# Kernel optimization log

Hardware: AMD Instinct MI355X
Metric: run time of the kernel (lower is better)

The kernel has to match this reference:

```python
import jax, jax.numpy as jnp
import numpy as np

B, S, D, H = 16, 2048, 1024, 1024

def setup_inputs() -> dict:
    key = jax.random.key(0)
    k1, k2, k3 = jax.random.split(key, 3)
    X = jax.random.normal(k1, (B, S, D), dtype=jnp.float32)
    W = jax.random.normal(k2, (3 * H, D), dtype=jnp.float32) * (1.0 / np.sqrt(D))
    b = jax.random.normal(k3, (3 * H,), dtype=jnp.float32) * 0.01
    return {"X": X, "W": W, "b": b}

def forget_mult(z, f):
    # z, f: [B, S, H]; h_t = z_t * f_t + (1 - f_t) * h_{t-1}, h_{-1} = 0
    z_t = jnp.moveaxis(z, 1, 0)  # [S, B, H]
    f_t = jnp.moveaxis(f, 1, 0)
    h0 = jnp.zeros(z.shape[::2], dtype=z.dtype)  # [B, H]
    def step(h, zf):
        zt, ft = zf
        h = zt * ft + (1.0 - ft) * h
        return h, h
    _, cs = jax.lax.scan(step, h0, (z_t, f_t))
    return jnp.moveaxis(cs, 0, 1)  # [B, S, H]

def reference(X, W, b):
    # window=1, output_gate=True, batch_first=True, zoneout=0, hidden=None
    Y = jnp.einsum('bsd,ed->bse', X, W) + b  # [B, S, 3H]
    z_gate, f_gate, o_gate = jnp.split(Y, 3, axis=2)
    z_gate = jnp.tanh(z_gate)
    f_gate = jax.nn.sigmoid(f_gate)
    c_gate = forget_mult(z_gate, f_gate)
    output = jax.nn.sigmoid(o_gate) * c_gate
    return output, c_gate[:, -1:]
```

## Files before the change

### kernel.cpp

```cpp
#include <hip/hip_runtime.h>
#include <hip/hip_bf16.h>
#include <hip/hip_fp16.h>


#define BB 16
#define SS 2048
#define DD 1024
#define HH 1024
#define N3 3072
#define CHUNK 64
#define NC (SS/CHUNK)

typedef _Float16 f16x8 __attribute__((ext_vector_type(8)));
typedef float    f32x4 __attribute__((ext_vector_type(4)));

__device__ __forceinline__ float sigm_f(float x) {
    return 1.0f / (1.0f + __expf(-x));
}
__device__ __forceinline__ float tanh_f(float x) {
    float ax = fabsf(x);
    float e  = __expf(2.0f * ax);
    float r  = 1.0f - 2.0f / (e + 1.0f);
    return copysignf(r, x);
}

__global__ __launch_bounds__(256) void cvt_f32_f16(
    const float* __restrict__ src, __half* __restrict__ dst, int n8)
{
    int i = blockIdx.x * 256 + threadIdx.x;
    if (i >= n8) return;
    const float4* s = (const float4*)src + (size_t)i * 2;
    float4 a = s[0], b = s[1];
    f16x8 v;
    v[0] = (_Float16)a.x; v[1] = (_Float16)a.y; v[2] = (_Float16)a.z; v[3] = (_Float16)a.w;
    v[4] = (_Float16)b.x; v[5] = (_Float16)b.y; v[6] = (_Float16)b.z; v[7] = (_Float16)b.w;
    *((f16x8*)dst + i) = v;
}

__global__ __launch_bounds__(256) void gemm_gates(
    const __half* __restrict__ Xs,
    const __half* __restrict__ W16,
    const float*  __restrict__ bias,
    __half* __restrict__ G)
{
    __shared__ __half As[128 * 32] __attribute__((aligned(16)));
    __shared__ __half Bs[128 * 32] __attribute__((aligned(16)));

    const int t  = threadIdx.x;
    const int w  = t >> 6;
    const int l  = t & 63;
    const int m0 = blockIdx.y * 128;
    const int n0 = blockIdx.x * 128;
    const int wm = w >> 1;
    const int wn = w & 1;

    f32x4 acc[4][4];
    #pragma unroll
    for (int m = 0; m < 4; ++m)
        #pragma unroll
        for (int n = 0; n < 4; ++n)
            acc[m][n] = f32x4{0.f, 0.f, 0.f, 0.f};

    const int c0 = w;
    const int c1 = w + 4;
    const int rA0 = c0 * 16 + (l >> 2);
    const int rA1 = c1 * 16 + (l >> 2);
    const int ck  = (l & 3) * 8;

    const __half* Xb = Xs + (size_t)m0 * DD;
    const __half* Wb = W16 + (size_t)n0 * DD;

    const int cl = l & 15;
    const int kg = l >> 4;

    for (int k0 = 0; k0 < DD; k0 += 32) {
        __builtin_amdgcn_global_load_lds(
            (const __attribute__((address_space(1))) void*)(Xb + (size_t)rA0 * DD + k0 + ck),
            (__attribute__((address_space(3))) void*)((char*)As + c0 * 1024), 16, 0, 0);
        __builtin_amdgcn_global_load_lds(
            (const __attribute__((address_space(1))) void*)(Xb + (size_t)rA1 * DD + k0 + ck),
            (__attribute__((address_space(3))) void*)((char*)As + c1 * 1024), 16, 0, 0);
        __builtin_amdgcn_global_load_lds(
            (const __attribute__((address_space(1))) void*)(Wb + (size_t)rA0 * DD + k0 + ck),
            (__attribute__((address_space(3))) void*)((char*)Bs + c0 * 1024), 16, 0, 0);
        __builtin_amdgcn_global_load_lds(
            (const __attribute__((address_space(1))) void*)(Wb + (size_t)rA1 * DD + k0 + ck),
            (__attribute__((address_space(3))) void*)((char*)Bs + c1 * 1024), 16, 0, 0);
        __syncthreads();

        f16x8 a[4], b[4];
        const f16x8* Av = (const f16x8*)As;
        const f16x8* Bv = (const f16x8*)Bs;
        #pragma unroll
        for (int m = 0; m < 4; ++m)
            a[m] = Av[(wm * 64 + m * 16 + cl) * 4 + kg];
        #pragma unroll
        for (int n = 0; n < 4; ++n)
            b[n] = Bv[(wn * 64 + n * 16 + cl) * 4 + kg];

        #pragma unroll
        for (int m = 0; m < 4; ++m)
            #pragma unroll
            for (int n = 0; n < 4; ++n)
                acc[m][n] = __builtin_amdgcn_mfma_f32_16x16x32_f16(
                    a[m], b[n], acc[m][n], 0, 0, 0);
        __syncthreads();
    }

    #pragma unroll
    for (int n = 0; n < 4; ++n) {
        const int gcol = n0 + wn * 64 + n * 16 + cl;
        const float bv = bias[gcol];
        #pragma unroll
        for (int m = 0; m < 4; ++m) {
            const int grow0 = m0 + wm * 64 + m * 16 + kg * 4;
            #pragma unroll
            for (int i = 0; i < 4; ++i) {
                G[(size_t)(grow0 + i) * N3 + gcol] = __float2half(acc[m][n][i] + bv);
            }
        }
    }
}

__global__ __launch_bounds__(256) void scan_pass1(
    const __half* __restrict__ G,
    float* __restrict__ Ac, float* __restrict__ Fc)
{
    const int flat = blockIdx.x * 256 + threadIdx.x;
    const int h  = flat & (HH - 1);
    const int c  = (flat >> 10) & (NC - 1);
    const int lb = flat >> 15;

    const __half* g = G + (size_t)(lb * SS + c * CHUNK) * N3 + h;
    float A = 0.f, F = 1.f;
    for (int s = 0; s < CHUNK; ++s) {
        float z = __half2float(g[0]);
        float f = __half2float(g[HH]);
        g += N3;
        float ft = sigm_f(f);
        float fp = 1.f - ft;
        A = tanh_f(z) * ft + fp * A;
        F *= fp;
    }
    Ac[flat] = A;
    Fc[flat] = F;
}

__global__ __launch_bounds__(256) void scan_pass2(
    const float* __restrict__ Ac, const float* __restrict__ Fc,
    float* __restrict__ Hin, float* __restrict__ c_last)
{
    const int flat = blockIdx.x * 256 + threadIdx.x;
    const int lb = flat >> 10;
    const int h  = flat & (HH - 1);
    float hc = 0.f;
    for (int c = 0; c < NC; ++c) {
        const size_t idx = (size_t)(lb * NC + c) * HH + h;
        Hin[idx] = hc;
        hc = Ac[idx] + Fc[idx] * hc;
    }
    c_last[flat] = hc;
}

__global__ __launch_bounds__(256) void scan_pass3(
    const __half* __restrict__ G, const float* __restrict__ Hin,
    float* __restrict__ out)
{
    const int flat = blockIdx.x * 256 + threadIdx.x;
    const int h  = flat & (HH - 1);
    const int c  = (flat >> 10) & (NC - 1);
    const int lb = flat >> 15;

    const __half* g = G + (size_t)(lb * SS + c * CHUNK) * N3 + h;
    float* o = out + (size_t)(lb * SS + c * CHUNK) * HH + h;
    float hc = Hin[flat];
    for (int s = 0; s < CHUNK; ++s) {
        float z  = __half2float(g[0]);
        float f  = __half2float(g[HH]);
        float og = __half2float(g[2 * HH]);
        g += N3;
        float ft = sigm_f(f);
        hc = tanh_f(z) * ft + (1.f - ft) * hc;
        *o = hc * sigm_f(og);
        o += HH;
    }
}

extern "C" void kernel_launch(void* const* d_in, const int* in_sizes, int n_in,
                              void* d_out, int out_size, void* d_ws, size_t ws_size,
                              hipStream_t stream) {
    const float* X    = (const float*)d_in[0];
    const float* W    = (const float*)d_in[1];
    const float* bias = (const float*)d_in[2];
    for (int i = 0; i < n_in && i < 3; ++i) {
        if      (in_sizes[i] == BB * SS * DD) X    = (const float*)d_in[i];
        else if (in_sizes[i] == N3 * DD)      W    = (const float*)d_in[i];
        else if (in_sizes[i] == N3)           bias = (const float*)d_in[i];
    }
    float* out = (float*)d_out;
    float* c_last_base = out + (size_t)BB * SS * HH;

    const size_t w16_b   = (size_t)N3 * DD * sizeof(__half);
    const size_t per_b_x = (size_t)SS * DD * sizeof(__half);
    const size_t per_b_g = (size_t)SS * N3 * sizeof(__half);
    const size_t per_b_s = (size_t)NC * HH * sizeof(float) * 3;
    int nb = 1;
    for (int cand = BB; cand >= 1; --cand) {
        if (w16_b + (size_t)cand * (per_b_x + per_b_g + per_b_s) <= ws_size) {
            nb = cand; break;
        }
    }

    __half* W16 = (__half*)d_ws;
    __half* X16 = (__half*)((char*)W16 + w16_b);
    __half* G   = (__half*)((char*)X16 + (size_t)nb * per_b_x);
    float*  Ac  = (float*)((char*)G + (size_t)nb * per_b_g);
    float*  Fc  = Ac + (size_t)nb * NC * HH;
    float*  Hin = Fc + (size_t)nb * NC * HH;

    {
        const int n8 = (N3 * DD) / 8;
        cvt_f32_f16<<<(n8 + 255) / 256, 256, 0, stream>>>(W, W16, n8);
    }

    for (int b0 = 0; b0 < BB; b0 += nb) {
        const int bs = (b0 + nb <= BB) ? nb : (BB - b0);

        const int n8x = (bs * SS * DD) / 8;
        cvt_f32_f16<<<(n8x + 255) / 256, 256, 0, stream>>>(
            X + (size_t)b0 * SS * DD, X16, n8x);

        dim3 gg(N3 / 128, bs * (SS / 128));
        gemm_gates<<<gg, 256, 0, stream>>>(X16, W16, bias, G);

        scan_pass1<<<(bs * NC * HH) / 256, 256, 0, stream>>>(G, Ac, Fc);
        scan_pass2<<<(bs * HH) / 256, 256, 0, stream>>>(Ac, Fc, Hin,
                                                        c_last_base + (size_t)b0 * HH);
        scan_pass3<<<(bs * NC * HH) / 256, 256, 0, stream>>>(G, Hin,
                                                             out + (size_t)b0 * SS * HH);
    }
}
```

Measured before the change: 425.6 us.

## Rewrite gate GEMM as 256x256x64 double-buffered 8-wave pipelined kernel

Replaces the 128x128x32 single-buffered GEMM with a 256x256 tile, BK=64, 512-thread kernel. It double-buffers LDS with async global-to-LDS loads that are split across phases, so the next tile's loads overlap the MFMA work. It also adds s_setprio, sched barriers and a swapped grid order so M-blocks vary fastest. The aim is to raise arithmetic intensity and hide memory latency in the dominant GEMM, at the cost of more LDS (128KB), more registers and reduced occupancy, plus a risk of LDS bank conflicts because the layout is unswizzled.

Measured after the change: 638.9 us. 50.1% more time.

```diff
diff --git a/kernel.cpp b/kernel.cpp
--- a/kernel.cpp
+++ b/kernel.cpp
@@ -10,6 +10,11 @@
 #define N3 3072
 #define CHUNK 64
 #define NC (SS/CHUNK)
+
+#define BM 256
+#define BN 256
+#define BK 64
+#define NKT (DD/BK)
 
 typedef _Float16 f16x8 __attribute__((ext_vector_type(8)));
 typedef float    f32x4 __attribute__((ext_vector_type(4)));
@@ -37,86 +42,120 @@
     *((f16x8*)dst + i) = v;
 }
 
-__global__ __launch_bounds__(256) void gemm_gates(
+__global__ __launch_bounds__(512) void gemm_gates8(
     const __half* __restrict__ Xs,
     const __half* __restrict__ W16,
     const float*  __restrict__ bias,
     __half* __restrict__ G)
 {
-    __shared__ __half As[128 * 32] __attribute__((aligned(16)));
-    __shared__ __half Bs[128 * 32] __attribute__((aligned(16)));
-
-    const int t  = threadIdx.x;
-    const int w  = t >> 6;
-    const int l  = t & 63;
-    const int m0 = blockIdx.y * 128;
-    const int n0 = blockIdx.x * 128;
-    const int wm = w >> 1;
-    const int wn = w & 1;
-
-    f32x4 acc[4][4];
+    __shared__ __half As[2][BM * BK] __attribute__((aligned(16)));
+    __shared__ __half Bs[2][BN * BK] __attribute__((aligned(16)));
+
+    const int t   = threadIdx.x;
+    const int wid = t >> 6;
+    const int l   = t & 63;
+    const int m0  = blockIdx.x * BM;
+    const int n0  = blockIdx.y * BN;
+    const int wr  = wid >> 2;
+    const int wc  = wid & 3;
+    const int cl  = l & 15;
+    const int kg  = l >> 4;
+
+    f32x4 acc[8][4];
     #pragma unroll
-    for (int m = 0; m < 4; ++m)
+    for (int m = 0; m < 8; ++m)
         #pragma unroll
         for (int n = 0; n < 4; ++n)
             acc[m][n] = f32x4{0.f, 0.f, 0.f, 0.f};
 
-    const int c0 = w;
-    const int c1 = w + 4;
-    const int rA0 = c0 * 16 + (l >> 2);
-    const int rA1 = c1 * 16 + (l >> 2);
-    const int ck  = (l & 3) * 8;
-
-    const __half* Xb = Xs + (size_t)m0 * DD;
-    const __half* Wb = W16 + (size_t)n0 * DD;
-
-    const int cl = l & 15;
-    const int kg = l >> 4;
-
-    for (int k0 = 0; k0 < DD; k0 += 32) {
-        __builtin_amdgcn_global_load_lds(
-            (const __attribute__((address_space(1))) void*)(Xb + (size_t)rA0 * DD + k0 + ck),
-            (__attribute__((address_space(3))) void*)((char*)As + c0 * 1024), 16, 0, 0);
-        __builtin_amdgcn_global_load_lds(
-            (const __attribute__((address_space(1))) void*)(Xb + (size_t)rA1 * DD + k0 + ck),
-            (__attribute__((address_space(3))) void*)((char*)As + c1 * 1024), 16, 0, 0);
-        __builtin_amdgcn_global_load_lds(
-            (const __attribute__((address_space(1))) void*)(Wb + (size_t)rA0 * DD + k0 + ck),
-            (__attribute__((address_space(3))) void*)((char*)Bs + c0 * 1024), 16, 0, 0);
-        __builtin_amdgcn_global_load_lds(
-            (const __attribute__((address_space(1))) void*)(Wb + (size_t)rA1 * DD + k0 + ck),
-            (__attribute__((address_space(3))) void*)((char*)Bs + c1 * 1024), 16, 0, 0);
-        __syncthreads();
-
-        f16x8 a[4], b[4];
-        const f16x8* Av = (const f16x8*)As;
-        const f16x8* Bv = (const f16x8*)Bs;
-        #pragma unroll
-        for (int m = 0; m < 4; ++m)
-            a[m] = Av[(wm * 64 + m * 16 + cl) * 4 + kg];
-        #pragma unroll
-        for (int n = 0; n < 4; ++n)
-            b[n] = Bv[(wn * 64 + n * 16 + cl) * 4 + kg];
-
-        #pragma unroll
-        for (int m = 0; m < 4; ++m)
-            #pragma unroll
-            for (int n = 0; n < 4; ++n)
-                acc[m][n] = __builtin_amdgcn_mfma_f32_16x16x32_f16(
-                    a[m], b[n], acc[m][n], 0, 0, 0);
-        __syncthreads();
-    }
+    const int srow = wid * 8 + (l >> 3);
+    const int scol = (l & 7) * 8;
+    const __half* Xb = Xs  + (size_t)(m0 + srow) * DD + scol;
+    const __half* Wb = W16 + (size_t)(n0 + srow) * DD + scol;
+
+#define ISSUE_A(slot, j, kt) \
+    __builtin_amdgcn_global_load_lds( \
+        (const __attribute__((address_space(1))) void*)(Xb + (size_t)(j) * 64 * DD + (kt) * BK), \
+        (__attribute__((address_space(3))) void*)(&As[slot][(j) * 4096 + wid * 512]), 16, 0, 0)
+#define ISSUE_B(slot, j, kt) \
+    __builtin_amdgcn_global_load_lds( \
+        (const __attribute__((address_space(1))) void*)(Wb + (size_t)(j) * 64 * DD + (kt) * BK), \
+        (__attribute__((address_space(3))) void*)(&Bs[slot][(j) * 4096 + wid * 512]), 16, 0, 0)
+
+#define PHASE(q, EXTRA) { \
+        const int rh = (q) >> 1, ch = (q) & 1; \
+        f16x8 a[4][2], b[2][2]; \
+        _Pragma("unroll") \
+        for (int i = 0; i < 4; ++i) \
+            _Pragma("unroll") \
+            for (int kh = 0; kh < 2; ++kh) \
+                a[i][kh] = *(const f16x8*)(Ab + ((wr * 128 + (rh * 4 + i) * 16 + cl) * BK + kh * 32 + kg * 8)); \
+        _Pragma("unroll") \
+        for (int j = 0; j < 2; ++j) \
+            _Pragma("unroll") \
+            for (int kh = 0; kh < 2; ++kh) \
+                b[j][kh] = *(const f16x8*)(Bb + ((wc * 64 + (ch * 2 + j) * 16 + cl) * BK + kh * 32 + kg * 8)); \
+        EXTRA; \
+        __builtin_amdgcn_s_barrier(); \
+        asm volatile("s_waitcnt lgkmcnt(0)" ::: "memory"); \
+        __builtin_amdgcn_sched_barrier(0); \
+        __builtin_amdgcn_s_setprio(1); \
+        _Pragma("unroll") \
+        for (int i = 0; i < 4; ++i) \
+            _Pragma("unroll") \
+            for (int j = 0; j < 2; ++j) \
+                _Pragma("unroll") \
+                for (int kh = 0; kh < 2; ++kh) \
+                    acc[rh * 4 + i][ch * 2 + j] = __builtin_amdgcn_mfma_f32_16x16x32_f16( \
+                        a[i][kh], b[j][kh], acc[rh * 4 + i][ch * 2 + j], 0, 0, 0); \
+        __builtin_amdgcn_s_setprio(0); \
+        __builtin_amdgcn_sched_barrier(0); \
+        __builtin_amdgcn_s_barrier(); \
+    }
+
+    ISSUE_A(0, 0, 0); ISSUE_A(0, 1, 0); ISSUE_A(0, 2, 0); ISSUE_A(0, 3, 0);
+    ISSUE_B(0, 0, 0); ISSUE_B(0, 1, 0); ISSUE_B(0, 2, 0); ISSUE_B(0, 3, 0);
+
+    for (int kt = 0; kt < NKT; ++kt) {
+        const int cur = kt & 1, nxt = cur ^ 1;
+        const __half* Ab = As[cur];
+        const __half* Bb = Bs[cur];
+
+        if (kt + 1 < NKT) {
+            ISSUE_A(nxt, 0, kt + 1); ISSUE_A(nxt, 1, kt + 1);
+            ISSUE_B(nxt, 0, kt + 1); ISSUE_B(nxt, 1, kt + 1);
+            asm volatile("s_waitcnt vmcnt(4)" ::: "memory");
+        } else {
+            asm volatile("s_waitcnt vmcnt(0)" ::: "memory");
+        }
+        __builtin_amdgcn_s_barrier();
+
+        PHASE(0, {});
+        if (kt + 1 < NKT) {
+            PHASE(1, {
+                ISSUE_A(nxt, 2, kt + 1); ISSUE_A(nxt, 3, kt + 1);
+                ISSUE_B(nxt, 2, kt + 1); ISSUE_B(nxt, 3, kt + 1);
+            });
+        } else {
+            PHASE(1, {});
+        }
+        PHASE(2, {});
+        PHASE(3, {});
+    }
+#undef PHASE
+#undef ISSUE_A
+#undef ISSUE_B
 
     #pragma unroll
-    for (int n = 0; n < 4; ++n) {
-        const int gcol = n0 + wn * 64 + n * 16 + cl;
+    for (int fc = 0; fc < 4; ++fc) {
+        const int gcol = n0 + wc * 64 + fc * 16 + cl;
         const float bv = bias[gcol];
         #pragma unroll
-        for (int m = 0; m < 4; ++m) {
-            const int grow0 = m0 + wm * 64 + m * 16 + kg * 4;
+        for (int fr = 0; fr < 8; ++fr) {
+            const int grow0 = m0 + wr * 128 + fr * 16 + kg * 4;
             #pragma unroll
             for (int i = 0; i < 4; ++i) {
-                G[(size_t)(grow0 + i) * N3 + gcol] = __float2half(acc[m][n][i] + bv);
+                G[(size_t)(grow0 + i) * N3 + gcol] = __float2half(acc[fr][fc][i] + bv);
             }
         }
     }
@@ -230,8 +269,8 @@
         cvt_f32_f16<<<(n8x + 255) / 256, 256, 0, stream>>>(
             X + (size_t)b0 * SS * DD, X16, n8x);
 
-        dim3 gg(N3 / 128, bs * (SS / 128));
-        gemm_gates<<<gg, 256, 0, stream>>>(X16, W16, bias, G);
+        dim3 gg(bs * (SS / BM), N3 / BN);
+        gemm_gates8<<<gg, 512, 0, stream>>>(X16, W16, bias, G);
 
         scan_pass1<<<(bs * NC * HH) / 256, 256, 0, stream>>>(G, Ac, Fc);
         scan_pass2<<<(bs * HH) / 256, 256, 0, stream>>>(Ac, Fc, Hin,
```

## Swizzle GEMM LDS layout, stage epilogue via LDS for coalesced stores, cap batch chunk

Applied to the files above, without the earlier changes.

The GEMM's LDS tile gets an XOR swizzle on the k-chunk position, applied both when global_load_lds writes it and when the MFMA fragments are read, to cut LDS bank conflicts. The epilogue now writes accumulators into a padded shared buffer and copies them out as 16-byte vector stores per row, replacing scattered 2-byte global writes. The batch chunk size is capped at 8, which keeps the intermediate buffers smaller and likely more cache-resident, at the cost of more kernel launches. The staged epilogue adds extra syncthreads rounds.

After: 450.1 us. +5.8%, slower.

```diff
diff --git a/kernel.cpp b/kernel.cpp
--- a/kernel.cpp
+++ b/kernel.cpp
@@ -43,8 +43,9 @@
     const float*  __restrict__ bias,
     __half* __restrict__ G)
 {
-    __shared__ __half As[128 * 32] __attribute__((aligned(16)));
-    __shared__ __half Bs[128 * 32] __attribute__((aligned(16)));
+    __shared__ __half smem[8192] __attribute__((aligned(16)));
+    __half* As = smem;
+    __half* Bs = smem + 4096;
 
     const int t  = threadIdx.x;
     const int w  = t >> 6;
@@ -53,6 +54,8 @@
     const int n0 = blockIdx.x * 128;
     const int wm = w >> 1;
     const int wn = w & 1;
+    const int cl = l & 15;
+    const int kg = l >> 4;
 
     f32x4 acc[4][4];
     #pragma unroll
@@ -65,13 +68,12 @@
     const int c1 = w + 4;
     const int rA0 = c0 * 16 + (l >> 2);
     const int rA1 = c1 * 16 + (l >> 2);
-    const int ck  = (l & 3) * 8;
-
-    const __half* Xb = Xs + (size_t)m0 * DD;
+    const int ck  = (((l & 3) ^ ((l >> 2) & 3) ^ ((l >> 4) & 3)) * 8);
+
+    const __half* Xb = Xs  + (size_t)m0 * DD;
     const __half* Wb = W16 + (size_t)n0 * DD;
 
-    const int cl = l & 15;
-    const int kg = l >> 4;
+    const int rpos = (kg ^ (cl & 3) ^ ((cl >> 2) & 3)) * 8;
 
     for (int k0 = 0; k0 < DD; k0 += 32) {
         __builtin_amdgcn_global_load_lds(
@@ -89,14 +91,12 @@
         __syncthreads();
 
         f16x8 a[4], b[4];
-        const f16x8* Av = (const f16x8*)As;
-        const f16x8* Bv = (const f16x8*)Bs;
         #pragma unroll
         for (int m = 0; m < 4; ++m)
-            a[m] = Av[(wm * 64 + m * 16 + cl) * 4 + kg];
+            a[m] = *(const f16x8*)(As + (wm * 64 + m * 16 + cl) * 32 + rpos);
         #pragma unroll
         for (int n = 0; n < 4; ++n)
-            b[n] = Bv[(wn * 64 + n * 16 + cl) * 4 + kg];
+            b[n] = *(const f16x8*)(Bs + (wn * 64 + n * 16 + cl) * 32 + rpos);
 
         #pragma unroll
         for (int m = 0; m < 4; ++m)
@@ -107,18 +107,39 @@
         __syncthreads();
     }
 
+    __half* sh = smem;
+    float bv[4];
     #pragma unroll
-    for (int n = 0; n < 4; ++n) {
-        const int gcol = n0 + wn * 64 + n * 16 + cl;
-        const float bv = bias[gcol];
-        #pragma unroll
-        for (int m = 0; m < 4; ++m) {
-            const int grow0 = m0 + wm * 64 + m * 16 + kg * 4;
+    for (int n = 0; n < 4; ++n) bv[n] = bias[n0 + wn * 64 + n * 16 + cl];
+
+    const int row_s = t >> 3;
+    const int chk   = t & 7;
+
+    #pragma unroll
+    for (int r = 0; r < 4; ++r) {
+        if (wm == (r >> 1)) {
             #pragma unroll
-            for (int i = 0; i < 4; ++i) {
-                G[(size_t)(grow0 + i) * N3 + gcol] = __float2half(acc[m][n][i] + bv);
+            for (int mm = 0; mm < 2; ++mm) {
+                const int m  = (r & 1) * 2 + mm;
+                const int rl = mm * 16 + kg * 4;
+                #pragma unroll
+                for (int n = 0; n < 4; ++n) {
+                    #pragma unroll
+                    for (int i = 0; i < 4; ++i) {
+                        sh[(rl + i) * 136 + wn * 64 + n * 16 + cl] =
+                            __float2half(acc[m][n][i] + bv[n]);
+                    }
+                }
             }
         }
+        __syncthreads();
+        {
+            const __half* src = sh + row_s * 136 + chk * 16;
+            __half* dst = G + (size_t)(m0 + r * 32 + row_s) * N3 + n0 + chk * 16;
+            *(f16x8*)(dst)     = *(const f16x8*)(src);
+            *(f16x8*)(dst + 8) = *(const f16x8*)(src + 8);
+        }
+        __syncthreads();
     }
 }
 
@@ -210,6 +231,7 @@
             nb = cand; break;
         }
     }
+    if (nb > 8) nb = 8;
 
     __half* W16 = (__half*)d_ws;
     __half* X16 = (__half*)((char*)W16 + w16_b);
```
